# Kernel tuning notes

Measured on AMD Instinct MI355X. Metric: run time of the kernel, lower is better.

Reference implementation:

```python
import jax, jax.numpy as jnp
import numpy as np

D = 512
K = 14            # 13 anomaly classes + 1 normal
NORMAL_IDX = K - 1
ALPHA = 0.2       # PLG alpha
THETA = 0.55      # PLG threshold
EPS = 1e-8


def _minmax(x, axis):
    mn = jnp.min(x, axis=axis, keepdims=True)
    mx = jnp.max(x, axis=axis, keepdims=True)
    return (x - mn) / (mx - mn + EPS)


def setup_inputs() -> dict:
    key = jax.random.key(0)
    k1, k2, k3, k4, k5 = jax.random.split(key, 5)
    B_n, B_a, F = 16, 16, 4096
    normal_feats = jax.random.normal(k1, (B_n, F, D), dtype=jnp.float32)
    anomaly_feats = jax.random.normal(k2, (B_a, F, D), dtype=jnp.float32)
    anomaly_class_idx = jax.random.randint(k3, (B_a,), 0, K - 1)  # in [0, K-2]
    # learned text prompt embeddings (output of PromptTextEncoder, pre-normalization)
    T_emb = jax.random.normal(k4, (K, D), dtype=jnp.float32)
    # stand-in temporal scoring head (TCSAL replaced by linear head; see notes)
    w_score = jax.random.normal(k5, (D,), dtype=jnp.float32) / np.sqrt(D)
    b_score = jnp.zeros((), dtype=jnp.float32)
    return {"normal_feats": normal_feats, "anomaly_feats": anomaly_feats,
            "anomaly_class_idx": anomaly_class_idx, "T_emb": T_emb,
            "w_score": w_score, "b_score": b_score}


def reference(normal_feats, anomaly_feats, anomaly_class_idx, T_emb, w_score, b_score):
    B_a, F_a, _ = anomaly_feats.shape
    # L2-normalized text embeddings (K, D)
    T = T_emb / (jnp.linalg.norm(T_emb, axis=-1, keepdims=True) + EPS)
    T_anomaly = T[:NORMAL_IDX]          # (K-1, D)
    T_n = T[NORMAL_IDX]                 # (D,)  use_nvp=False -> T_n_enhanced = T_n
    T_n_enhanced = T_n

    # dense similarities
    S_nn = jnp.einsum('bfd,d->bf', normal_feats, T_n_enhanced)      # (B_n, F_n)
    phi_na = jnp.einsum('bfd,kd->bfk', normal_feats, T_anomaly)     # (B_n, F_n, K-1)
    S_an = jnp.einsum('bfd,d->bf', anomaly_feats, T_n_enhanced)     # (B_a, F_a)

    # per-sample true-class gather + matmul (vectorized: gather class vec then contract)
    T_true = T_anomaly[anomaly_class_idx]                            # (B_a, D)
    S_aa_true = jnp.einsum('bfd,bd->bf', anomaly_feats, T_true)      # (B_a, F_a)

    # 'other classes' similarities: exclude tau[b] per sample.
    # Since exactly one class is excluded, max_other = K-2 statically.
    phi_all = jnp.einsum('bfd,kd->bfk', anomaly_feats, T_anomaly)    # (B_a, F_a, K-1)
    j = jnp.arange(K - 2)                                            # (K-2,)
    other_idx = jnp.where(j[None, :] < anomaly_class_idx[:, None], j[None, :], j[None, :] + 1)  # (B_a, K-2)
    phi_aa_other = jnp.take_along_axis(
        phi_all, jnp.broadcast_to(other_idx[:, None, :], (B_a, F_a, K - 2)), axis=2)

    # pseudo-label generator (alpha-fused, normality-guided, thresholded)
    s_aa = _minmax(S_aa_true, axis=1)
    s_an = _minmax(S_an, axis=1)
    fused = (1.0 - ALPHA) * s_aa + ALPHA * (1.0 - s_an)
    pseudo_labels = (fused > THETA).astype(jnp.float32)

    # temporal scores (linear head stand-in for TCSAL)
    scores = jax.nn.sigmoid(jnp.einsum('bfd,d->bf', anomaly_feats, w_score) + b_score)

    S_aa_norm = _minmax(S_aa_true, axis=1)
    return (S_nn, phi_na, S_an, S_aa_true, phi_aa_other, S_aa_norm,
            pseudo_labels, scores, T_n_enhanced)
```

## Files before the change

### kernel.cpp

```cpp
#include <hip/hip_runtime.h>
#include <math.h>

#define D 512
#define K 14
#define EPS 1e-8f

#define O_SNN       0
#define O_PHINA     65536
#define O_SAN       917504
#define O_SAA       983040
#define O_PHIOTHER  1048576
#define O_SAANORM   1835008
#define O_PSEUDO    1900544
#define O_SCORES    1966080
#define O_TN        2031616

__device__ __forceinline__ float wave_sum(float v) {
    v += __shfl_xor(v, 1);
    v += __shfl_xor(v, 2);
    v += __shfl_xor(v, 4);
    v += __shfl_xor(v, 8);
    v += __shfl_xor(v, 16);
    v += __shfl_xor(v, 32);
    return v;
}

__device__ __forceinline__ float wave_min(float v) {
    v = fminf(v, __shfl_xor(v, 1));
    v = fminf(v, __shfl_xor(v, 2));
    v = fminf(v, __shfl_xor(v, 4));
    v = fminf(v, __shfl_xor(v, 8));
    v = fminf(v, __shfl_xor(v, 16));
    v = fminf(v, __shfl_xor(v, 32));
    return v;
}
__device__ __forceinline__ float wave_max(float v) {
    v = fmaxf(v, __shfl_xor(v, 1));
    v = fmaxf(v, __shfl_xor(v, 2));
    v = fmaxf(v, __shfl_xor(v, 4));
    v = fmaxf(v, __shfl_xor(v, 8));
    v = fmaxf(v, __shfl_xor(v, 16));
    v = fmaxf(v, __shfl_xor(v, 32));
    return v;
}

__global__ __launch_bounds__(960) void kprep(const float* __restrict__ T_emb,
                                             const float* __restrict__ w_score,
                                             float* __restrict__ W,
                                             float* __restrict__ tn_out) {
    int lane = threadIdx.x & 63;
    int w = threadIdx.x >> 6;
    float4* W4 = (float4*)W;
    if (w < K) {
        const float4* src = (const float4*)T_emb + w * 128;
        float4 a = src[lane];
        float4 b = src[64 + lane];
        float ss = a.x * a.x + a.y * a.y + a.z * a.z + a.w * a.w
                 + b.x * b.x + b.y * b.y + b.z * b.z + b.w * b.w;
        ss = wave_sum(ss);
        float inv = 1.0f / (sqrtf(ss) + EPS);
        float4 na = make_float4(a.x * inv, a.y * inv, a.z * inv, a.w * inv);
        float4 nb = make_float4(b.x * inv, b.y * inv, b.z * inv, b.w * inv);
        W4[w * 128 + lane] = na;
        W4[w * 128 + 64 + lane] = nb;
        if (w == K - 1) {
            float4* t4 = (float4*)tn_out;
            t4[lane] = na;
            t4[64 + lane] = nb;
        }
    } else {
        const float4* src = (const float4*)w_score;
        W4[14 * 128 + lane] = src[lane];
        W4[14 * 128 + 64 + lane] = src[64 + lane];
    }
}

__global__ __launch_bounds__(256) void knormal(const float4* __restrict__ feats,
                                               const float4* __restrict__ W4,
                                               float* __restrict__ S_nn,
                                               float* __restrict__ phi_na,
                                               int nrows) {
    int lane = threadIdx.x & 63;
    int wave = (blockIdx.x * 256 + threadIdx.x) >> 6;
    int nwaves = (gridDim.x * 256) >> 6;

    float4 t0[K], t1[K];
#pragma unroll
    for (int k = 0; k < K; k++) {
        t0[k] = W4[k * 128 + lane];
        t1[k] = W4[k * 128 + 64 + lane];
    }

    for (int row = wave; row < nrows; row += nwaves) {
        float4 f0 = feats[row * 128 + lane];
        float4 f1 = feats[row * 128 + 64 + lane];
        float acc[K];
#pragma unroll
        for (int k = 0; k < K; k++) {
            float a = f0.x * t0[k].x + f0.y * t0[k].y + f0.z * t0[k].z + f0.w * t0[k].w
                    + f1.x * t1[k].x + f1.y * t1[k].y + f1.z * t1[k].z + f1.w * t1[k].w;
            acc[k] = wave_sum(a);
        }
        float val = acc[0];
#pragma unroll
        for (int k = 1; k < K; k++) val = (lane == k) ? acc[k] : val;
        if (lane < 14) {
            float* ptr = (lane < 13) ? (phi_na + row * 13 + lane) : (S_nn + row);
            *ptr = val;
        }
    }
}

__global__ __launch_bounds__(256) void kanom(const float4* __restrict__ feats,
                                             const float4* __restrict__ W4,
                                             const int* __restrict__ cls,
                                             const float* __restrict__ b_score,
                                             float* __restrict__ S_an,
                                             float* __restrict__ S_aa,
                                             float* __restrict__ phi_other,
                                             float* __restrict__ scores,
                                             int nrows) {
    const int NK = 15;
    int lane = threadIdx.x & 63;
    int wave = (blockIdx.x * 256 + threadIdx.x) >> 6;
    int nwaves = (gridDim.x * 256) >> 6;

    float4 t0[NK], t1[NK];
#pragma unroll
    for (int k = 0; k < NK; k++) {
        t0[k] = W4[k * 128 + lane];
        t1[k] = W4[k * 128 + 64 + lane];
    }
    float bsc = *b_score;

    for (int row = wave; row < nrows; row += nwaves) {
        int b = row >> 12;
        int ci = cls[b];
        float4 f0 = feats[row * 128 + lane];
        float4 f1 = feats[row * 128 + 64 + lane];
        float acc[NK];
#pragma unroll
        for (int k = 0; k < NK; k++) {
            float a = f0.x * t0[k].x + f0.y * t0[k].y + f0.z * t0[k].z + f0.w * t0[k].w
                    + f1.x * t1[k].x + f1.y * t1[k].y + f1.z * t1[k].z + f1.w * t1[k].w;
            acc[k] = wave_sum(a);
        }
        int sel;
        if (lane < 12) sel = (lane < ci) ? lane : lane + 1;
        else if (lane == 13) sel = ci;
        else sel = 0;

        float val = acc[0];
#pragma unroll
        for (int k = 1; k < 13; k++) val = (sel == k) ? acc[k] : val;
        if (lane == 12) val = acc[13];
        if (lane == 14) val = 1.0f / (1.0f + expf(-(acc[14] + bsc)));

        if (lane < 15) {
            float* ptr;
            if (lane < 12)       ptr = phi_other + row * 12 + lane;
            else if (lane == 12) ptr = S_an + row;
            else if (lane == 13) ptr = S_aa + row;
            else                 ptr = scores + row;
            *ptr = val;
        }
    }
}

__global__ __launch_bounds__(256) void kminmax(const float* __restrict__ S_aa,
                                               const float* __restrict__ S_an,
                                               float* __restrict__ mm) {
    int b = blockIdx.x;
    int t = threadIdx.x;
    int lane = t & 63, wid = t >> 6;
    const float* pa = S_aa + b * 4096;
    const float* pn = S_an + b * 4096;
    float mnA = 1e30f, mxA = -1e30f, mnN = 1e30f, mxN = -1e30f;
    for (int i = t; i < 4096; i += 256) {
        float a = pa[i];
        float n = pn[i];
        mnA = fminf(mnA, a); mxA = fmaxf(mxA, a);
        mnN = fminf(mnN, n); mxN = fmaxf(mxN, n);
    }
    mnA = wave_min(mnA); mxA = wave_max(mxA);
    mnN = wave_min(mnN); mxN = wave_max(mxN);
    __shared__ float red[4][4];
    if (lane == 0) {
        red[wid][0] = mnA; red[wid][1] = mxA;
        red[wid][2] = mnN; red[wid][3] = mxN;
    }
    __syncthreads();
    if (t == 0) {
        float a0 = red[0][0], a1 = red[0][1], a2 = red[0][2], a3 = red[0][3];
        for (int w = 1; w < 4; w++) {
            a0 = fminf(a0, red[w][0]); a1 = fmaxf(a1, red[w][1]);
            a2 = fminf(a2, red[w][2]); a3 = fmaxf(a3, red[w][3]);
        }
        mm[b * 4 + 0] = a0; mm[b * 4 + 1] = a1;
        mm[b * 4 + 2] = a2; mm[b * 4 + 3] = a3;
    }
}

__global__ __launch_bounds__(256) void kfinal(const float* __restrict__ S_aa,
                                              const float* __restrict__ S_an,
                                              const float* __restrict__ mm,
                                              float* __restrict__ S_aa_norm,
                                              float* __restrict__ pseudo) {
    int i = blockIdx.x * 256 + threadIdx.x;
    if (i >= 65536) return;
    int b = i >> 12;
    float mnA = mm[b * 4 + 0], mxA = mm[b * 4 + 1];
    float mnN = mm[b * 4 + 2], mxN = mm[b * 4 + 3];
    float s_aa = (S_aa[i] - mnA) / (mxA - mnA + EPS);
    float s_an = (S_an[i] - mnN) / (mxN - mnN + EPS);
    float fused = 0.8f * s_aa + 0.2f * (1.0f - s_an);
    pseudo[i] = fused > 0.55f ? 1.0f : 0.0f;
    S_aa_norm[i] = s_aa;
}

extern "C" void kernel_launch(void* const* d_in, const int* in_sizes, int n_in,
                              void* d_out, int out_size, void* d_ws, size_t ws_size,
                              hipStream_t stream) {
    const float* normal_feats  = (const float*)d_in[0];
    const float* anomaly_feats = (const float*)d_in[1];
    const int*   cls           = (const int*)d_in[2];
    const float* T_emb         = (const float*)d_in[3];
    const float* w_score       = (const float*)d_in[4];
    const float* b_score       = (const float*)d_in[5];
    float* out = (float*)d_out;

    float* W  = (float*)d_ws;
    float* mm = (float*)d_ws + 15 * 512;

    const int nrows = 16 * 4096;

    kprep<<<1, 960, 0, stream>>>(T_emb, w_score, W, out + O_TN);

    knormal<<<1024, 256, 0, stream>>>((const float4*)normal_feats, (const float4*)W,
                                      out + O_SNN, out + O_PHINA, nrows);

    kanom<<<1024, 256, 0, stream>>>((const float4*)anomaly_feats, (const float4*)W,
                                    cls, b_score,
                                    out + O_SAN, out + O_SAA, out + O_PHIOTHER,
                                    out + O_SCORES, nrows);

    kminmax<<<16, 256, 0, stream>>>(out + O_SAA, out + O_SAN, mm);

    kfinal<<<256, 256, 0, stream>>>(out + O_SAA, out + O_SAN, mm,
                                    out + O_SAANORM, out + O_PSEUDO);
}
```

Measured before the change: 356.2 us.

## Use transpose-style multi-reduction and prefetch next row in similarity kernels

Replaces per-class full wave butterfly reductions (14-15 separate 6-step shuffles) with a recursive-halving multi-value reduction across 16 values, so each lane ends up holding one class's sum in bit-reversed order. It also software-prefetches the next row's features into registers while computing the current row, and adds a launch-bounds occupancy hint. This cuts shuffle count substantially and overlaps memory latency, at the cost of extra registers and more complex output index mapping.

```diff
diff --git a/kernel.cpp b/kernel.cpp
--- a/kernel.cpp
+++ b/kernel.cpp
@@ -24,7 +24,6 @@
     v += __shfl_xor(v, 32);
     return v;
 }
-
 __device__ __forceinline__ float wave_min(float v) {
     v = fminf(v, __shfl_xor(v, 1));
     v = fminf(v, __shfl_xor(v, 2));
@@ -42,6 +41,29 @@
     v = fmaxf(v, __shfl_xor(v, 16));
     v = fmaxf(v, __shfl_xor(v, 32));
     return v;
+}
+
+__device__ __forceinline__ float multi_reduce16(float (&vals)[16], int lane) {
+#pragma unroll
+    for (int s = 0; s < 4; s++) {
+        const int half = 8 >> s;
+        const bool sel = (lane >> s) & 1;
+#pragma unroll
+        for (int i = 0; i < half; i++) {
+            float lo = vals[i], hi = vals[i + half];
+            float a = sel ? lo : hi;
+            float b = __shfl_xor(a, 1 << s);
+            vals[i] = sel ? (hi + b) : (lo + b);
+        }
+    }
+    float v = vals[0];
+    v += __shfl_xor(v, 16);
+    v += __shfl_xor(v, 32);
+    return v;
+}
+
+__device__ __forceinline__ int bitrev4(int x) {
+    return ((x & 1) << 3) | ((x & 2) << 1) | ((x & 4) >> 1) | ((x & 8) >> 3);
 }
 
 __global__ __launch_bounds__(960) void kprep(const float* __restrict__ T_emb,
@@ -75,11 +97,11 @@
     }
 }
 
-__global__ __launch_bounds__(256) void knormal(const float4* __restrict__ feats,
-                                               const float4* __restrict__ W4,
-                                               float* __restrict__ S_nn,
-                                               float* __restrict__ phi_na,
-                                               int nrows) {
+__global__ __launch_bounds__(256, 2) void knormal(const float4* __restrict__ feats,
+                                                  const float4* __restrict__ W4,
+                                                  float* __restrict__ S_nn,
+                                                  float* __restrict__ phi_na,
+                                                  int nrows) {
     int lane = threadIdx.x & 63;
     int wave = (blockIdx.x * 256 + threadIdx.x) >> 6;
     int nwaves = (gridDim.x * 256) >> 6;
@@ -90,36 +112,43 @@
         t0[k] = W4[k * 128 + lane];
         t1[k] = W4[k * 128 + 64 + lane];
     }
-
-    for (int row = wave; row < nrows; row += nwaves) {
-        float4 f0 = feats[row * 128 + lane];
-        float4 f1 = feats[row * 128 + 64 + lane];
-        float acc[K];
+    const int myk = bitrev4(lane);
+
+    int row = wave;
+    float4 f0 = feats[row * 128 + lane];
+    float4 f1 = feats[row * 128 + 64 + lane];
+    while (row < nrows) {
+        int nrow = row + nwaves;
+        float4 g0, g1;
+        if (nrow < nrows) {
+            g0 = feats[nrow * 128 + lane];
+            g1 = feats[nrow * 128 + 64 + lane];
+        }
+        float vals[16];
 #pragma unroll
         for (int k = 0; k < K; k++) {
-            float a = f0.x * t0[k].x + f0.y * t0[k].y + f0.z * t0[k].z + f0.w * t0[k].w
+            vals[k] = f0.x * t0[k].x + f0.y * t0[k].y + f0.z * t0[k].z + f0.w * t0[k].w
                     + f1.x * t1[k].x + f1.y * t1[k].y + f1.z * t1[k].z + f1.w * t1[k].w;
-            acc[k] = wave_sum(a);
-        }
-        float val = acc[0];
-#pragma unroll
-        for (int k = 1; k < K; k++) val = (lane == k) ? acc[k] : val;
-        if (lane < 14) {
-            float* ptr = (lane < 13) ? (phi_na + row * 13 + lane) : (S_nn + row);
-            *ptr = val;
-        }
-    }
-}
-
-__global__ __launch_bounds__(256) void kanom(const float4* __restrict__ feats,
-                                             const float4* __restrict__ W4,
-                                             const int* __restrict__ cls,
-                                             const float* __restrict__ b_score,
-                                             float* __restrict__ S_an,
-                                             float* __restrict__ S_aa,
-                                             float* __restrict__ phi_other,
-                                             float* __restrict__ scores,
-                                             int nrows) {
+        }
+        vals[14] = 0.0f; vals[15] = 0.0f;
+        float v = multi_reduce16(vals, lane);
+        if (lane < 16 && myk < 14) {
+            float* ptr = (myk < 13) ? (phi_na + row * 13 + myk) : (S_nn + row);
+            *ptr = v;
+        }
+        row = nrow; f0 = g0; f1 = g1;
+    }
+}
+
+__global__ __launch_bounds__(256, 2) void kanom(const float4* __restrict__ feats,
+                                                const float4* __restrict__ W4,
+                                                const int* __restrict__ cls,
+                                                const float* __restrict__ b_score,
+                                                float* __restrict__ S_an,
+                                                float* __restrict__ S_aa,
+                                                float* __restrict__ phi_other,
+                                                float* __restrict__ scores,
+                                                int nrows) {
     const int NK = 15;
     int lane = threadIdx.x & 63;
     int wave = (blockIdx.x * 256 + threadIdx.x) >> 6;
@@ -132,38 +161,42 @@
         t1[k] = W4[k * 128 + 64 + lane];
     }
     float bsc = *b_score;
-
-    for (int row = wave; row < nrows; row += nwaves) {
-        int b = row >> 12;
-        int ci = cls[b];
-        float4 f0 = feats[row * 128 + lane];
-        float4 f1 = feats[row * 128 + 64 + lane];
-        float acc[NK];
+    const int myk = bitrev4(lane);
+
+    int row = wave;
+    float4 f0 = feats[row * 128 + lane];
+    float4 f1 = feats[row * 128 + 64 + lane];
+    while (row < nrows) {
+        int nrow = row + nwaves;
+        float4 g0, g1;
+        if (nrow < nrows) {
+            g0 = feats[nrow * 128 + lane];
+            g1 = feats[nrow * 128 + 64 + lane];
+        }
+        int ci = cls[row >> 12];
+        float vals[16];
 #pragma unroll
         for (int k = 0; k < NK; k++) {
-            float a = f0.x * t0[k].x + f0.y * t0[k].y + f0.z * t0[k].z + f0.w * t0[k].w
+            vals[k] = f0.x * t0[k].x + f0.y * t0[k].y + f0.z * t0[k].z + f0.w * t0[k].w
                     + f1.x * t1[k].x + f1.y * t1[k].y + f1.z * t1[k].z + f1.w * t1[k].w;
-            acc[k] = wave_sum(a);
-        }
-        int sel;
-        if (lane < 12) sel = (lane < ci) ? lane : lane + 1;
-        else if (lane == 13) sel = ci;
-        else sel = 0;
-
-        float val = acc[0];
-#pragma unroll
-        for (int k = 1; k < 13; k++) val = (sel == k) ? acc[k] : val;
-        if (lane == 12) val = acc[13];
-        if (lane == 14) val = 1.0f / (1.0f + expf(-(acc[14] + bsc)));
-
-        if (lane < 15) {
+        }
+        vals[15] = 0.0f;
+        float v = multi_reduce16(vals, lane);
+        if (lane < 16 && myk < 15) {
             float* ptr;
-            if (lane < 12)       ptr = phi_other + row * 12 + lane;
-            else if (lane == 12) ptr = S_an + row;
-            else if (lane == 13) ptr = S_aa + row;
-            else                 ptr = scores + row;
+            float val = v;
+            if (myk < 13) {
+                if (myk == ci) ptr = S_aa + row;
+                else           ptr = phi_other + row * 12 + ((myk < ci) ? myk : myk - 1);
+            } else if (myk == 13) {
+                ptr = S_an + row;
+            } else {
+                ptr = scores + row;
+                val = 1.0f / (1.0f + expf(-(v + bsc)));
+            }
             *ptr = val;
         }
+        row = nrow; f0 = g0; f1 = g1;
     }
 }
 
```

Result: faster. 324.3 us (-9.0%).

## Switch to one-thread-per-row dot products with split-D partials and post kernels

Applied to the files above, without the earlier changes.

Replaces the wave-per-row kernels, which reduced each of 14–15 dot products with cross-lane shuffles, with a kernel where each thread accumulates all class dot products for one row over half of D. The weights become wave-uniform scalar loads. Two partial-sum planes are written to workspace, and small post kernels combine them and apply the class gather and sigmoid. This is meant to remove the shuffle-reduction cost. In exchange, each lane reads a different row with a large stride, so memory access is no longer coalesced across the wave. It also adds an extra round trip through workspace memory and two extra kernel launches.

```diff
diff --git a/kernel.cpp b/kernel.cpp
--- a/kernel.cpp
+++ b/kernel.cpp
@@ -4,6 +4,7 @@
 #define D 512
 #define K 14
 #define EPS 1e-8f
+#define NROWS 65536
 
 #define O_SNN       0
 #define O_PHINA     65536
@@ -24,7 +25,6 @@
     v += __shfl_xor(v, 32);
     return v;
 }
-
 __device__ __forceinline__ float wave_min(float v) {
     v = fminf(v, __shfl_xor(v, 1));
     v = fminf(v, __shfl_xor(v, 2));
@@ -75,95 +75,69 @@
     }
 }
 
-__global__ __launch_bounds__(256) void knormal(const float4* __restrict__ feats,
-                                               const float4* __restrict__ W4,
-                                               float* __restrict__ S_nn,
-                                               float* __restrict__ phi_na,
-                                               int nrows) {
-    int lane = threadIdx.x & 63;
-    int wave = (blockIdx.x * 256 + threadIdx.x) >> 6;
-    int nwaves = (gridDim.x * 256) >> 6;
-
-    float4 t0[K], t1[K];
+template<int NK>
+__global__ __launch_bounds__(256) void kdots(const float4* __restrict__ feats,
+                                             const float4* __restrict__ W4,
+                                             float* __restrict__ wsd) {
+    const int lane = threadIdx.x & 63;
+    const int wid  = threadIdx.x >> 6;
+    const int row  = blockIdx.x * 256 + wid * 64 + lane;
+    const int half = blockIdx.y;
+    const int kb   = half * 64;
+
+    const float4* fp = feats + (size_t)row * 128 + kb;
+    const float4* tp = W4 + kb;
+
+    float acc[NK];
 #pragma unroll
-    for (int k = 0; k < K; k++) {
-        t0[k] = W4[k * 128 + lane];
-        t1[k] = W4[k * 128 + 64 + lane];
-    }
-
-    for (int row = wave; row < nrows; row += nwaves) {
-        float4 f0 = feats[row * 128 + lane];
-        float4 f1 = feats[row * 128 + 64 + lane];
-        float acc[K];
+    for (int j = 0; j < NK; j++) acc[j] = 0.0f;
+
+#pragma unroll 4
+    for (int s = 0; s < 64; s++) {
+        float4 f = fp[s];
+        int su = __builtin_amdgcn_readfirstlane(s);
 #pragma unroll
-        for (int k = 0; k < K; k++) {
-            float a = f0.x * t0[k].x + f0.y * t0[k].y + f0.z * t0[k].z + f0.w * t0[k].w
-                    + f1.x * t1[k].x + f1.y * t1[k].y + f1.z * t1[k].z + f1.w * t1[k].w;
-            acc[k] = wave_sum(a);
+        for (int j = 0; j < NK; j++) {
+            float4 t = tp[j * 128 + su];
+            acc[j] = fmaf(f.x, t.x, fmaf(f.y, t.y, fmaf(f.z, t.z, fmaf(f.w, t.w, acc[j]))));
         }
-        float val = acc[0];
-#pragma unroll
-        for (int k = 1; k < K; k++) val = (lane == k) ? acc[k] : val;
-        if (lane < 14) {
-            float* ptr = (lane < 13) ? (phi_na + row * 13 + lane) : (S_nn + row);
-            *ptr = val;
-        }
-    }
-}
-
-__global__ __launch_bounds__(256) void kanom(const float4* __restrict__ feats,
-                                             const float4* __restrict__ W4,
-                                             const int* __restrict__ cls,
-                                             const float* __restrict__ b_score,
-                                             float* __restrict__ S_an,
-                                             float* __restrict__ S_aa,
-                                             float* __restrict__ phi_other,
-                                             float* __restrict__ scores,
-                                             int nrows) {
-    const int NK = 15;
-    int lane = threadIdx.x & 63;
-    int wave = (blockIdx.x * 256 + threadIdx.x) >> 6;
-    int nwaves = (gridDim.x * 256) >> 6;
-
-    float4 t0[NK], t1[NK];
-#pragma unroll
-    for (int k = 0; k < NK; k++) {
-        t0[k] = W4[k * 128 + lane];
-        t1[k] = W4[k * 128 + 64 + lane];
-    }
-    float bsc = *b_score;
-
-    for (int row = wave; row < nrows; row += nwaves) {
-        int b = row >> 12;
-        int ci = cls[b];
-        float4 f0 = feats[row * 128 + lane];
-        float4 f1 = feats[row * 128 + 64 + lane];
-        float acc[NK];
-#pragma unroll
-        for (int k = 0; k < NK; k++) {
-            float a = f0.x * t0[k].x + f0.y * t0[k].y + f0.z * t0[k].z + f0.w * t0[k].w
-                    + f1.x * t1[k].x + f1.y * t1[k].y + f1.z * t1[k].z + f1.w * t1[k].w;
-            acc[k] = wave_sum(a);
-        }
-        int sel;
-        if (lane < 12) sel = (lane < ci) ? lane : lane + 1;
-        else if (lane == 13) sel = ci;
-        else sel = 0;
-
-        float val = acc[0];
-#pragma unroll
-        for (int k = 1; k < 13; k++) val = (sel == k) ? acc[k] : val;
-        if (lane == 12) val = acc[13];
-        if (lane == 14) val = 1.0f / (1.0f + expf(-(acc[14] + bsc)));
-
-        if (lane < 15) {
-            float* ptr;
-            if (lane < 12)       ptr = phi_other + row * 12 + lane;
-            else if (lane == 12) ptr = S_an + row;
-            else if (lane == 13) ptr = S_aa + row;
-            else                 ptr = scores + row;
-            *ptr = val;
-        }
+    }
+
+    float4* o = (float4*)(wsd + ((size_t)half * NROWS + row) * 16);
+    o[0] = make_float4(acc[0], acc[1], acc[2],  acc[3]);
+    o[1] = make_float4(acc[4], acc[5], acc[6],  acc[7]);
+    o[2] = make_float4(acc[8], acc[9], acc[10], acc[11]);
+    o[3] = make_float4(acc[12], acc[13], (NK > 14) ? acc[14] : 0.0f, 0.0f);
+}
+
+__global__ __launch_bounds__(256) void kpostN(const float* __restrict__ wsd,
+                                              float* __restrict__ S_nn,
+                                              float* __restrict__ phi_na) {
+    int i = blockIdx.x * 256 + threadIdx.x;
+    int row = i >> 4, j = i & 15;
+    float v = wsd[i] + wsd[NROWS * 16 + i];
+    if (j < 13)       phi_na[row * 13 + j] = v;
+    else if (j == 13) S_nn[row] = v;
+}
+
+__global__ __launch_bounds__(256) void kpostA(const float* __restrict__ wsd,
+                                              const int* __restrict__ cls,
+                                              const float* __restrict__ b_score,
+                                              float* __restrict__ S_an,
+                                              float* __restrict__ S_aa,
+                                              float* __restrict__ phi_other,
+                                              float* __restrict__ scores) {
+    int i = blockIdx.x * 256 + threadIdx.x;
+    int row = i >> 4, j = i & 15;
+    float v = wsd[i] + wsd[NROWS * 16 + i];
+    int ci = cls[row >> 12];
+    if (j < 13) {
+        if (j == ci) S_aa[row] = v;
+        else         phi_other[row * 12 + ((j < ci) ? j : j - 1)] = v;
+    } else if (j == 13) {
+        S_an[row] = v;
+    } else if (j == 14) {
+        scores[row] = 1.0f / (1.0f + expf(-(v + b_score[0])));
     }
 }
 
@@ -207,7 +181,7 @@
                                               float* __restrict__ S_aa_norm,
                                               float* __restrict__ pseudo) {
     int i = blockIdx.x * 256 + threadIdx.x;
-    if (i >= 65536) return;
+    if (i >= NROWS) return;
     int b = i >> 12;
     float mnA = mm[b * 4 + 0], mxA = mm[b * 4 + 1];
     float mnN = mm[b * 4 + 2], mxN = mm[b * 4 + 3];
@@ -229,20 +203,23 @@
     const float* b_score       = (const float*)d_in[5];
     float* out = (float*)d_out;
 
-    float* W  = (float*)d_ws;
-    float* mm = (float*)d_ws + 15 * 512;
-
-    const int nrows = 16 * 4096;
+    float* W     = (float*)d_ws;
+    float* mm    = (float*)d_ws + 8192;
+    float* dotsN = (float*)d_ws + 8192 + 64;
+    float* dotsA = dotsN + 2 * NROWS * 16;
 
     kprep<<<1, 960, 0, stream>>>(T_emb, w_score, W, out + O_TN);
 
-    knormal<<<1024, 256, 0, stream>>>((const float4*)normal_feats, (const float4*)W,
-                                      out + O_SNN, out + O_PHINA, nrows);
-
-    kanom<<<1024, 256, 0, stream>>>((const float4*)anomaly_feats, (const float4*)W,
-                                    cls, b_score,
-                                    out + O_SAN, out + O_SAA, out + O_PHIOTHER,
-                                    out + O_SCORES, nrows);
+    dim3 gdots(256, 2);
+    kdots<14><<<gdots, 256, 0, stream>>>((const float4*)normal_feats,
+                                         (const float4*)W, dotsN);
+    kpostN<<<(NROWS * 16) / 256, 256, 0, stream>>>(dotsN, out + O_SNN, out + O_PHINA);
+
+    kdots<15><<<gdots, 256, 0, stream>>>((const float4*)anomaly_feats,
+                                         (const float4*)W, dotsA);
+    kpostA<<<(NROWS * 16) / 256, 256, 0, stream>>>(dotsA, cls, b_score,
+                                                   out + O_SAN, out + O_SAA,
+                                                   out + O_PHIOTHER, out + O_SCORES);
 
     kminmax<<<16, 256, 0, stream>>>(out + O_SAA, out + O_SAN, mm);
 
```

Result: no change. 352.5 us (-1.0%).
